# Optimization experiments

Hardware: AMD Instinct MI355X
Metric: run time of the kernel (lower is better)

## Reference

```python
import jax, jax.numpy as jnp
import numpy as np


def setup_inputs() -> dict:
    key = jax.random.key(0)
    k0, k1, k2, k3 = jax.random.split(key, 4)
    B, T, C, H = 4, 4096, 1024, 64
    input_val = jax.random.normal(k0, (B, T, C), dtype=jnp.float32)
    scale = 0.02
    Wq = jax.random.normal(k1, (H, C), dtype=jnp.float32) * scale
    Wk = jax.random.normal(k2, (H, C), dtype=jnp.float32) * scale
    Wv = jax.random.normal(k3, (H, C), dtype=jnp.float32) * scale
    k_mask = jnp.ones((B, T), dtype=jnp.int32)
    return {"input_val": input_val, "Wq": Wq, "Wk": Wk, "Wv": Wv, "k_mask": k_mask}


def reference(input_val, Wq, Wk, Wv, k_mask):
    # input_val: [B, T, C]; Wq/Wk/Wv: [H, C] (torch Linear weight layout)
    B, T, C = input_val.shape
    H = Wq.shape[0]
    Q = input_val @ Wq.T  # [B, T, H]
    K = input_val @ Wk.T  # [B, T, H]
    V = input_val @ Wv.T  # [B, T, H]
    att = jnp.einsum('bqh,bkh->bqk', Q, K) / jnp.sqrt(jnp.asarray(H, input_val.dtype))
    neg_inf = jnp.asarray(-jnp.inf, att.dtype)
    # padding mask over keys: [B, 1, T]
    att = jnp.where(k_mask[:, None, :] == 0, neg_inf, att)
    # causal mask (rebuilt each call in the original)
    causal = jnp.tril(jnp.ones((T, T), dtype=bool))
    att = jnp.where(causal[None, :, :], att, neg_inf)
    att = jax.nn.softmax(att, axis=-1)
    return att @ V  # [B, T, H]
```

## Files before the change

### kernel.cpp

```cpp
#include <hip/hip_runtime.h>

typedef unsigned short u16;
typedef unsigned int u32;
typedef __attribute__((ext_vector_type(4))) float f32x4;
typedef __attribute__((ext_vector_type(8))) short s16x8;
typedef __attribute__((ext_vector_type(4))) int i32x4;
typedef __attribute__((ext_vector_type(2))) u32 u32x2;
typedef __attribute__((ext_vector_type(4))) u32 u32x4;

#define TT 4096
#define NEG_BIG (-3.0e38f)

__device__ __forceinline__ u16 f2bf(float x){
  u32 u = __builtin_bit_cast(u32, x);
  u32 r = (u + 0x7FFFu + ((u >> 16) & 1u)) >> 16;
  return (u16)r;
}
__device__ __forceinline__ u32 pk2(float a, float b){
  return (u32)f2bf(a) | ((u32)f2bf(b) << 16);
}
__device__ __forceinline__ f32x4 mfma16(s16x8 a, s16x8 b, f32x4 c){
  return __builtin_amdgcn_mfma_f32_16x16x32_bf16(a, b, c, 0, 0, 0);
}

__global__ __launch_bounds__(256) void wconv_k(const float* __restrict__ Wq,
                                               const float* __restrict__ Wk,
                                               const float* __restrict__ Wv,
                                               u16* __restrict__ Wb){
  int i = blockIdx.x * 256 + threadIdx.x;
  float v;
  if (i < 65536)       v = Wq[i] * 0.125f;
  else if (i < 131072) v = Wk[i - 65536];
  else                 v = Wv[i - 131072];
  Wb[i] = f2bf(v);
}

__global__ __launch_bounds__(256) void qkv_k(const float* __restrict__ X,
                                             const u16* __restrict__ Wb,
                                             u16* __restrict__ Qb,
                                             u16* __restrict__ Kb,
                                             u16* __restrict__ Vt){
  __shared__ u16 Xs[64][40];
  const int tid = threadIdx.x;
  const int lane = tid & 63;
  const int wid = tid >> 6;
  const int q4 = lane & 15, g = lane >> 4;
  const int row0 = blockIdx.x * 64;
  const int b = row0 >> 12;
  const int trow = row0 & 4095;
  const int srow = tid >> 2, spart = tid & 3;
  const float* xsrc = X + (size_t)(row0 + srow) * 1024 + spart * 8;
  f32x4 c0 = *(const f32x4*)(xsrc);
  f32x4 c1 = *(const f32x4*)(xsrc + 4);
  f32x4 acc[3][4];
  #pragma unroll
  for (int ci = 0; ci < 3; ++ci)
    #pragma unroll
    for (int tt = 0; tt < 4; ++tt) acc[ci][tt] = (f32x4){0.f, 0.f, 0.f, 0.f};
  const int ct0 = wid * 3;

  for (int kc = 0; kc < 32; ++kc){
    s16x8 wf[3];
    #pragma unroll
    for (int ci = 0; ci < 3; ++ci){
      int ct = ct0 + ci;
      wf[ci] = *(const s16x8*)(Wb + (size_t)(ct * 16 + q4) * 1024 + kc * 32 + g * 8);
    }
    const float* nx = xsrc + (kc < 31 ? (kc + 1) * 32 : 0);
    f32x4 n0 = *(const f32x4*)(nx);
    f32x4 n1 = *(const f32x4*)(nx + 4);
    u32x4 wv;
    wv[0] = pk2(c0[0], c0[1]); wv[1] = pk2(c0[2], c0[3]);
    wv[2] = pk2(c1[0], c1[1]); wv[3] = pk2(c1[2], c1[3]);
    *(u32x4*)&Xs[srow][spart * 8] = wv;
    __syncthreads();
    s16x8 xf[4];
    #pragma unroll
    for (int tt = 0; tt < 4; ++tt) xf[tt] = *(const s16x8*)&Xs[tt * 16 + q4][g * 8];
    #pragma unroll
    for (int ci = 0; ci < 3; ++ci){
      #pragma unroll
      for (int tt = 0; tt < 4; ++tt){
        if (ct0 + ci < 8) acc[ci][tt] = mfma16(wf[ci], xf[tt], acc[ci][tt]);
        else              acc[ci][tt] = mfma16(xf[tt], wf[ci], acc[ci][tt]);
      }
    }
    __syncthreads();
    c0 = n0; c1 = n1;
  }
  #pragma unroll
  for (int ci = 0; ci < 3; ++ci){
    int ct = ct0 + ci;
    #pragma unroll
    for (int tt = 0; tt < 4; ++tt){
      f32x4 v = acc[ci][tt];
      u32x2 pw; pw[0] = pk2(v[0], v[1]); pw[1] = pk2(v[2], v[3]);
      if (ct < 8){
        u16* dst = (ct < 4 ? Qb : Kb) + (size_t)(row0 + tt * 16 + q4) * 64 + (ct & 3) * 16 + g * 4;
        *(u32x2*)dst = pw;
      } else {
        u16* dst = Vt + (size_t)(b * 64 + (ct - 8) * 16 + q4) * TT + trow + tt * 16 + g * 4;
        *(u32x2*)dst = pw;
      }
    }
  }
}

__global__ __launch_bounds__(128) void attn_k(const u16* __restrict__ Qb,
                                              const u16* __restrict__ Kb,
                                              const u16* __restrict__ Vt,
                                              const int* __restrict__ km,
                                              float* __restrict__ out){
  __shared__ u16 Plds[2][16][72];
  __shared__ float Part[2][16][64];
  __shared__ float Pml[2][2][16];
  const int tid = threadIdx.x;
  const int wid = tid >> 6;
  const int lane = tid & 63;
  const int q4 = lane & 15, g = lane >> 4;
  const int b = blockIdx.x >> 7;
  const int p = blockIdx.x & 127;
  float mK, lK; f32x4 oK[4];

  #pragma unroll
  for (int si = 0; si < 2; ++si){
    const int s = (si == 0) ? p : 255 - p;
    const int qbase = s * 16;
    const int q_lane = qbase + q4;
    const int ntiles = (s >> 2) + 1;
    const int t0 = (ntiles * wid) >> 1;
    const int t1 = (ntiles * (wid + 1)) >> 1;
    const u16* qptr = Qb + (size_t)(b * TT + qbase + q4) * 64 + g * 8;
    const s16x8 qf0 = *(const s16x8*)(qptr);
    const s16x8 qf1 = *(const s16x8*)(qptr + 32);
    float m = NEG_BIG, l = 0.f;
    f32x4 o[4];
    #pragma unroll
    for (int ht = 0; ht < 4; ++ht) o[ht] = (f32x4){0.f, 0.f, 0.f, 0.f};

    for (int kt = t0; kt < t1; ++kt){
      const int kb = kt * 64;
      const u16* kp = Kb + (size_t)(b * TT + kb + q4) * 64 + g * 8;
      s16x8 kf[4][2];
      #pragma unroll
      for (int mt = 0; mt < 4; ++mt){
        kf[mt][0] = *(const s16x8*)(kp + mt * 1024);
        kf[mt][1] = *(const s16x8*)(kp + mt * 1024 + 32);
      }
      f32x4 sA[4];
      #pragma unroll
      for (int mt = 0; mt < 4; ++mt){
        sA[mt] = mfma16(kf[mt][0], qf0, (f32x4){0.f, 0.f, 0.f, 0.f});
        sA[mt] = mfma16(kf[mt][1], qf1, sA[mt]);
      }
      #pragma unroll
      for (int mt = 0; mt < 4; ++mt){
        i32x4 mk = *(const i32x4*)(km + b * TT + kb + mt * 16 + g * 4);
        #pragma unroll
        for (int r = 0; r < 4; ++r) if (mk[r] == 0) sA[mt][r] = NEG_BIG;
      }
      if (kt == ntiles - 1){
        #pragma unroll
        for (int mt = 0; mt < 4; ++mt)
          #pragma unroll
          for (int r = 0; r < 4; ++r){
            int key = kb + mt * 16 + g * 4 + r;
            if (key > q_lane) sA[mt][r] = NEG_BIG;
          }
      }
      float vmax = NEG_BIG;
      #pragma unroll
      for (int mt = 0; mt < 4; ++mt)
        #pragma unroll
        for (int r = 0; r < 4; ++r) vmax = fmaxf(vmax, sA[mt][r]);
      vmax = fmaxf(vmax, __shfl_xor(vmax, 16));
      vmax = fmaxf(vmax, __shfl_xor(vmax, 32));
      const float mn = fmaxf(m, vmax);
      const float sc = __expf(m - mn);
      float ps = 0.f;
      float pvv[4][4];
      #pragma unroll
      for (int mt = 0; mt < 4; ++mt)
        #pragma unroll
        for (int r = 0; r < 4; ++r){
          float e = __expf(sA[mt][r] - mn);
          pvv[mt][r] = e; ps += e;
        }
      ps += __shfl_xor(ps, 16);
      ps += __shfl_xor(ps, 32);
      l = l * sc + ps;
      m = mn;
      #pragma unroll
      for (int ht = 0; ht < 4; ++ht) o[ht] *= sc;
      #pragma unroll
      for (int mt = 0; mt < 4; ++mt){
        u32x2 pw; pw[0] = pk2(pvv[mt][0], pvv[mt][1]); pw[1] = pk2(pvv[mt][2], pvv[mt][3]);
        *(u32x2*)&Plds[wid][q4][mt * 16 + g * 4] = pw;
      }
      const s16x8 pf0 = *(const s16x8*)&Plds[wid][q4][g * 8];
      const s16x8 pf1 = *(const s16x8*)&Plds[wid][q4][32 + g * 8];
      const u16* vp = Vt + (size_t)(b * 64 + q4) * TT + kb + g * 8;
      #pragma unroll
      for (int ht = 0; ht < 4; ++ht){
        s16x8 vf0 = *(const s16x8*)(vp + (size_t)(ht * 16) * TT);
        s16x8 vf1 = *(const s16x8*)(vp + (size_t)(ht * 16) * TT + 32);
        o[ht] = mfma16(vf0, pf0, o[ht]);
        o[ht] = mfma16(vf1, pf1, o[ht]);
      }
    }
    if (si != wid){
      #pragma unroll
      for (int ht = 0; ht < 4; ++ht) *(f32x4*)&Part[si][q4][ht * 16 + g * 4] = o[ht];
      if (g == 0){ Pml[si][0][q4] = m; Pml[si][1][q4] = l; }
    } else {
      mK = m; lK = l;
      #pragma unroll
      for (int ht = 0; ht < 4; ++ht) oK[ht] = o[ht];
    }
  }
  __syncthreads();
  const int s = (wid == 0) ? p : 255 - p;
  const float m1 = Pml[wid][0][q4], l1 = Pml[wid][1][q4];
  const float mt_ = fmaxf(mK, m1);
  const float a = __expf(mK - mt_), bb = __expf(m1 - mt_);
  const float lt = lK * a + l1 * bb;
  const float rl = 1.0f / lt;
  float* op = out + (size_t)(b * TT + s * 16 + q4) * 64;
  #pragma unroll
  for (int ht = 0; ht < 4; ++ht){
    f32x4 o1 = *(const f32x4*)&Part[wid][q4][ht * 16 + g * 4];
    f32x4 ov;
    #pragma unroll
    for (int r = 0; r < 4; ++r) ov[r] = (oK[ht][r] * a + o1[r] * bb) * rl;
    *(f32x4*)(op + ht * 16 + g * 4) = ov;
  }
}

extern "C" void kernel_launch(void* const* d_in, const int* in_sizes, int n_in,
                              void* d_out, int out_size, void* d_ws, size_t ws_size,
                              hipStream_t stream){
  const float* X  = (const float*)d_in[0];
  const float* Wq = (const float*)d_in[1];
  const float* Wk = (const float*)d_in[2];
  const float* Wv = (const float*)d_in[3];
  const int*   km = (const int*)d_in[4];
  float* out = (float*)d_out;
  u16* Qb = (u16*)d_ws;
  u16* Kb = Qb + (size_t)16384 * 64;
  u16* Vt = Kb + (size_t)16384 * 64;
  u16* Wb = Vt + (size_t)16384 * 64;
  hipLaunchKernelGGL(wconv_k, dim3(768), dim3(256), 0, stream, Wq, Wk, Wv, Wb);
  hipLaunchKernelGGL(qkv_k,   dim3(256), dim3(256), 0, stream, X, Wb, Qb, Kb, Vt);
  hipLaunchKernelGGL(attn_k,  dim3(512), dim3(128), 0, stream, Qb, Kb, Vt, km, out);
}
```

Measured before the change: 223.2 us.

## Split attention key range across 8 waves and halve QKV row tile

The attention kernel now runs 8 waves per block: each of the two query strips is split over 4 waves that each take a quarter of the causal key tiles, and the four partial softmax states are merged through LDS. Previously 2 waves each processed both strips sequentially. The QKV projection kernel processes 32 rows per block instead of 64, doubling its grid to 512 blocks. Both changes aim to raise parallelism and occupancy on the many-CU GPU, at the cost of more LDS, a larger merge step, and less reuse of weight fragments per block in the projection.

After: 192.5 us. 13.8% less time.

```diff
diff --git a/kernel.cpp b/kernel.cpp
--- a/kernel.cpp
+++ b/kernel.cpp
@@ -6,7 +6,6 @@
 typedef __attribute__((ext_vector_type(8))) short s16x8;
 typedef __attribute__((ext_vector_type(4))) int i32x4;
 typedef __attribute__((ext_vector_type(2))) u32 u32x2;
-typedef __attribute__((ext_vector_type(4))) u32 u32x4;
 
 #define TT 4096
 #define NEG_BIG (-3.0e38f)
@@ -40,23 +39,22 @@
                                              u16* __restrict__ Qb,
                                              u16* __restrict__ Kb,
                                              u16* __restrict__ Vt){
-  __shared__ u16 Xs[64][40];
+  __shared__ u16 Xs[32][40];
   const int tid = threadIdx.x;
   const int lane = tid & 63;
   const int wid = tid >> 6;
   const int q4 = lane & 15, g = lane >> 4;
-  const int row0 = blockIdx.x * 64;
+  const int row0 = blockIdx.x * 32;
   const int b = row0 >> 12;
   const int trow = row0 & 4095;
-  const int srow = tid >> 2, spart = tid & 3;
-  const float* xsrc = X + (size_t)(row0 + srow) * 1024 + spart * 8;
+  const int srow = tid >> 3, spart = tid & 7;
+  const float* xsrc = X + (size_t)(row0 + srow) * 1024 + spart * 4;
   f32x4 c0 = *(const f32x4*)(xsrc);
-  f32x4 c1 = *(const f32x4*)(xsrc + 4);
-  f32x4 acc[3][4];
+  f32x4 acc[3][2];
   #pragma unroll
   for (int ci = 0; ci < 3; ++ci)
     #pragma unroll
-    for (int tt = 0; tt < 4; ++tt) acc[ci][tt] = (f32x4){0.f, 0.f, 0.f, 0.f};
+    for (int tt = 0; tt < 2; ++tt) acc[ci][tt] = (f32x4){0.f, 0.f, 0.f, 0.f};
   const int ct0 = wid * 3;
 
   for (int kc = 0; kc < 32; ++kc){
@@ -68,31 +66,29 @@
     }
     const float* nx = xsrc + (kc < 31 ? (kc + 1) * 32 : 0);
     f32x4 n0 = *(const f32x4*)(nx);
-    f32x4 n1 = *(const f32x4*)(nx + 4);
-    u32x4 wv;
+    u32x2 wv;
     wv[0] = pk2(c0[0], c0[1]); wv[1] = pk2(c0[2], c0[3]);
-    wv[2] = pk2(c1[0], c1[1]); wv[3] = pk2(c1[2], c1[3]);
-    *(u32x4*)&Xs[srow][spart * 8] = wv;
+    *(u32x2*)&Xs[srow][spart * 4] = wv;
     __syncthreads();
-    s16x8 xf[4];
-    #pragma unroll
-    for (int tt = 0; tt < 4; ++tt) xf[tt] = *(const s16x8*)&Xs[tt * 16 + q4][g * 8];
+    s16x8 xf[2];
+    #pragma unroll
+    for (int tt = 0; tt < 2; ++tt) xf[tt] = *(const s16x8*)&Xs[tt * 16 + q4][g * 8];
     #pragma unroll
     for (int ci = 0; ci < 3; ++ci){
       #pragma unroll
-      for (int tt = 0; tt < 4; ++tt){
+      for (int tt = 0; tt < 2; ++tt){
         if (ct0 + ci < 8) acc[ci][tt] = mfma16(wf[ci], xf[tt], acc[ci][tt]);
         else              acc[ci][tt] = mfma16(xf[tt], wf[ci], acc[ci][tt]);
       }
     }
     __syncthreads();
-    c0 = n0; c1 = n1;
+    c0 = n0;
   }
   #pragma unroll
   for (int ci = 0; ci < 3; ++ci){
     int ct = ct0 + ci;
     #pragma unroll
-    for (int tt = 0; tt < 4; ++tt){
+    for (int tt = 0; tt < 2; ++tt){
       f32x4 v = acc[ci][tt];
       u32x2 pw; pw[0] = pk2(v[0], v[1]); pw[1] = pk2(v[2], v[3]);
       if (ct < 8){
@@ -106,133 +102,127 @@
   }
 }
 
-__global__ __launch_bounds__(128) void attn_k(const u16* __restrict__ Qb,
-                                              const u16* __restrict__ Kb,
-                                              const u16* __restrict__ Vt,
-                                              const int* __restrict__ km,
-                                              float* __restrict__ out){
-  __shared__ u16 Plds[2][16][72];
-  __shared__ float Part[2][16][64];
-  __shared__ float Pml[2][2][16];
+__global__ __launch_bounds__(512, 4) void attn_k(const u16* __restrict__ Qb,
+                                                 const u16* __restrict__ Kb,
+                                                 const u16* __restrict__ Vt,
+                                                 const int* __restrict__ km,
+                                                 float* __restrict__ out){
+  __shared__ u16 Plds[8][16][72];
+  __shared__ float Part[2][4][16][68];
+  __shared__ float Pml[2][4][2][16];
   const int tid = threadIdx.x;
   const int wid = tid >> 6;
   const int lane = tid & 63;
   const int q4 = lane & 15, g = lane >> 4;
   const int b = blockIdx.x >> 7;
   const int p = blockIdx.x & 127;
-  float mK, lK; f32x4 oK[4];
-
-  #pragma unroll
-  for (int si = 0; si < 2; ++si){
-    const int s = (si == 0) ? p : 255 - p;
-    const int qbase = s * 16;
-    const int q_lane = qbase + q4;
-    const int ntiles = (s >> 2) + 1;
-    const int t0 = (ntiles * wid) >> 1;
-    const int t1 = (ntiles * (wid + 1)) >> 1;
-    const u16* qptr = Qb + (size_t)(b * TT + qbase + q4) * 64 + g * 8;
-    const s16x8 qf0 = *(const s16x8*)(qptr);
-    const s16x8 qf1 = *(const s16x8*)(qptr + 32);
-    float m = NEG_BIG, l = 0.f;
-    f32x4 o[4];
-    #pragma unroll
-    for (int ht = 0; ht < 4; ++ht) o[ht] = (f32x4){0.f, 0.f, 0.f, 0.f};
-
-    for (int kt = t0; kt < t1; ++kt){
-      const int kb = kt * 64;
-      const u16* kp = Kb + (size_t)(b * TT + kb + q4) * 64 + g * 8;
-      s16x8 kf[4][2];
-      #pragma unroll
-      for (int mt = 0; mt < 4; ++mt){
-        kf[mt][0] = *(const s16x8*)(kp + mt * 1024);
-        kf[mt][1] = *(const s16x8*)(kp + mt * 1024 + 32);
-      }
-      f32x4 sA[4];
-      #pragma unroll
-      for (int mt = 0; mt < 4; ++mt){
-        sA[mt] = mfma16(kf[mt][0], qf0, (f32x4){0.f, 0.f, 0.f, 0.f});
-        sA[mt] = mfma16(kf[mt][1], qf1, sA[mt]);
-      }
-      #pragma unroll
-      for (int mt = 0; mt < 4; ++mt){
-        i32x4 mk = *(const i32x4*)(km + b * TT + kb + mt * 16 + g * 4);
-        #pragma unroll
-        for (int r = 0; r < 4; ++r) if (mk[r] == 0) sA[mt][r] = NEG_BIG;
-      }
-      if (kt == ntiles - 1){
-        #pragma unroll
-        for (int mt = 0; mt < 4; ++mt)
-          #pragma unroll
-          for (int r = 0; r < 4; ++r){
-            int key = kb + mt * 16 + g * 4 + r;
-            if (key > q_lane) sA[mt][r] = NEG_BIG;
-          }
-      }
-      float vmax = NEG_BIG;
-      #pragma unroll
-      for (int mt = 0; mt < 4; ++mt)
-        #pragma unroll
-        for (int r = 0; r < 4; ++r) vmax = fmaxf(vmax, sA[mt][r]);
-      vmax = fmaxf(vmax, __shfl_xor(vmax, 16));
-      vmax = fmaxf(vmax, __shfl_xor(vmax, 32));
-      const float mn = fmaxf(m, vmax);
-      const float sc = __expf(m - mn);
-      float ps = 0.f;
-      float pvv[4][4];
+  const int si = wid & 1;
+  const int qt = wid >> 1;
+
+  const int s = (si == 0) ? p : 255 - p;
+  const int qbase = s * 16;
+  const int q_lane = qbase + q4;
+  const int ntiles = (s >> 2) + 1;
+  const int t0 = (ntiles * qt) >> 2;
+  const int t1 = (ntiles * (qt + 1)) >> 2;
+  const u16* qptr = Qb + (size_t)(b * TT + qbase + q4) * 64 + g * 8;
+  const s16x8 qf0 = *(const s16x8*)(qptr);
+  const s16x8 qf1 = *(const s16x8*)(qptr + 32);
+  float m = NEG_BIG, l = 0.f;
+  f32x4 o[4];
+  #pragma unroll
+  for (int ht = 0; ht < 4; ++ht) o[ht] = (f32x4){0.f, 0.f, 0.f, 0.f};
+
+  for (int kt = t0; kt < t1; ++kt){
+    const int kb = kt * 64;
+    const u16* kp = Kb + (size_t)(b * TT + kb + q4) * 64 + g * 8;
+    s16x8 kf[4][2];
+    #pragma unroll
+    for (int mt = 0; mt < 4; ++mt){
+      kf[mt][0] = *(const s16x8*)(kp + mt * 1024);
+      kf[mt][1] = *(const s16x8*)(kp + mt * 1024 + 32);
+    }
+    f32x4 sA[4];
+    #pragma unroll
+    for (int mt = 0; mt < 4; ++mt){
+      sA[mt] = mfma16(kf[mt][0], qf0, (f32x4){0.f, 0.f, 0.f, 0.f});
+      sA[mt] = mfma16(kf[mt][1], qf1, sA[mt]);
+    }
+    #pragma unroll
+    for (int mt = 0; mt < 4; ++mt){
+      i32x4 mk = *(const i32x4*)(km + b * TT + kb + mt * 16 + g * 4);
+      #pragma unroll
+      for (int r = 0; r < 4; ++r) if (mk[r] == 0) sA[mt][r] = NEG_BIG;
+    }
+    if (kt == ntiles - 1){
       #pragma unroll
       for (int mt = 0; mt < 4; ++mt)
         #pragma unroll
         for (int r = 0; r < 4; ++r){
-          float e = __expf(sA[mt][r] - mn);
-          pvv[mt][r] = e; ps += e;
+          int key = kb + mt * 16 + g * 4 + r;
+          if (key > q_lane) sA[mt][r] = NEG_BIG;
         }
-      ps += __shfl_xor(ps, 16);
-      ps += __shfl_xor(ps, 32);
-      l = l * sc + ps;
-      m = mn;
-      #pragma unroll
-      for (int ht = 0; ht < 4; ++ht) o[ht] *= sc;
-      #pragma unroll
-      for (int mt = 0; mt < 4; ++mt){
-        u32x2 pw; pw[0] = pk2(pvv[mt][0], pvv[mt][1]); pw[1] = pk2(pvv[mt][2], pvv[mt][3]);
-        *(u32x2*)&Plds[wid][q4][mt * 16 + g * 4] = pw;
-      }
-      const s16x8 pf0 = *(const s16x8*)&Plds[wid][q4][g * 8];
-      const s16x8 pf1 = *(const s16x8*)&Plds[wid][q4][32 + g * 8];
-      const u16* vp = Vt + (size_t)(b * 64 + q4) * TT + kb + g * 8;
-      #pragma unroll
-      for (int ht = 0; ht < 4; ++ht){
-        s16x8 vf0 = *(const s16x8*)(vp + (size_t)(ht * 16) * TT);
-        s16x8 vf1 = *(const s16x8*)(vp + (size_t)(ht * 16) * TT + 32);
-        o[ht] = mfma16(vf0, pf0, o[ht]);
-        o[ht] = mfma16(vf1, pf1, o[ht]);
-      }
-    }
-    if (si != wid){
-      #pragma unroll
-      for (int ht = 0; ht < 4; ++ht) *(f32x4*)&Part[si][q4][ht * 16 + g * 4] = o[ht];
-      if (g == 0){ Pml[si][0][q4] = m; Pml[si][1][q4] = l; }
-    } else {
-      mK = m; lK = l;
-      #pragma unroll
-      for (int ht = 0; ht < 4; ++ht) oK[ht] = o[ht];
-    }
-  }
+    }
+    float vmax = NEG_BIG;
+    #pragma unroll
+    for (int mt = 0; mt < 4; ++mt)
+      #pragma unroll
+      for (int r = 0; r < 4; ++r) vmax = fmaxf(vmax, sA[mt][r]);
+    vmax = fmaxf(vmax, __shfl_xor(vmax, 16));
+    vmax = fmaxf(vmax, __shfl_xor(vmax, 32));
+    const float mn = fmaxf(m, vmax);
+    const float sc = __expf(m - mn);
+    float ps = 0.f;
+    #pragma unroll
+    for (int mt = 0; mt < 4; ++mt){
+      float e0 = __expf(sA[mt][0] - mn), e1 = __expf(sA[mt][1] - mn);
+      float e2 = __expf(sA[mt][2] - mn), e3 = __expf(sA[mt][3] - mn);
+      ps += (e0 + e1) + (e2 + e3);
+      u32x2 pw; pw[0] = pk2(e0, e1); pw[1] = pk2(e2, e3);
+      *(u32x2*)&Plds[wid][q4][mt * 16 + g * 4] = pw;
+    }
+    ps += __shfl_xor(ps, 16);
+    ps += __shfl_xor(ps, 32);
+    l = l * sc + ps;
+    m = mn;
+    #pragma unroll
+    for (int ht = 0; ht < 4; ++ht) o[ht] *= sc;
+    const s16x8 pf0 = *(const s16x8*)&Plds[wid][q4][g * 8];
+    const s16x8 pf1 = *(const s16x8*)&Plds[wid][q4][32 + g * 8];
+    const u16* vp = Vt + (size_t)(b * 64 + q4) * TT + kb + g * 8;
+    #pragma unroll
+    for (int ht = 0; ht < 4; ++ht){
+      s16x8 vf0 = *(const s16x8*)(vp + (size_t)(ht * 16) * TT);
+      s16x8 vf1 = *(const s16x8*)(vp + (size_t)(ht * 16) * TT + 32);
+      o[ht] = mfma16(vf0, pf0, o[ht]);
+      o[ht] = mfma16(vf1, pf1, o[ht]);
+    }
+  }
+  #pragma unroll
+  for (int ht = 0; ht < 4; ++ht) *(f32x4*)&Part[si][qt][q4][ht * 16 + g * 4] = o[ht];
+  if (g == 0){ Pml[si][qt][0][q4] = m; Pml[si][qt][1][q4] = l; }
   __syncthreads();
-  const int s = (wid == 0) ? p : 255 - p;
-  const float m1 = Pml[wid][0][q4], l1 = Pml[wid][1][q4];
-  const float mt_ = fmaxf(mK, m1);
-  const float a = __expf(mK - mt_), bb = __expf(m1 - mt_);
-  const float lt = lK * a + l1 * bb;
-  const float rl = 1.0f / lt;
-  float* op = out + (size_t)(b * TT + s * 16 + q4) * 64;
-  #pragma unroll
-  for (int ht = 0; ht < 4; ++ht){
-    f32x4 o1 = *(const f32x4*)&Part[wid][q4][ht * 16 + g * 4];
-    f32x4 ov;
-    #pragma unroll
-    for (int r = 0; r < 4; ++r) ov[r] = (oK[ht][r] * a + o1[r] * bb) * rl;
-    *(f32x4*)(op + ht * 16 + g * 4) = ov;
+  if (wid < 2){
+    const int so = (wid == 0) ? p : 255 - p;
+    float mm0 = Pml[wid][0][0][q4], mm1 = Pml[wid][1][0][q4];
+    float mm2 = Pml[wid][2][0][q4], mm3 = Pml[wid][3][0][q4];
+    float ll0 = Pml[wid][0][1][q4], ll1 = Pml[wid][1][1][q4];
+    float ll2 = Pml[wid][2][1][q4], ll3 = Pml[wid][3][1][q4];
+    const float mt_ = fmaxf(fmaxf(mm0, mm1), fmaxf(mm2, mm3));
+    const float w0 = __expf(mm0 - mt_), w1 = __expf(mm1 - mt_);
+    const float w2 = __expf(mm2 - mt_), w3 = __expf(mm3 - mt_);
+    const float lt = ll0 * w0 + ll1 * w1 + ll2 * w2 + ll3 * w3;
+    const float rl = 1.0f / lt;
+    float* op = out + (size_t)(b * TT + so * 16 + q4) * 64;
+    #pragma unroll
+    for (int ht = 0; ht < 4; ++ht){
+      f32x4 o0 = *(const f32x4*)&Part[wid][0][q4][ht * 16 + g * 4];
+      f32x4 o1 = *(const f32x4*)&Part[wid][1][q4][ht * 16 + g * 4];
+      f32x4 o2 = *(const f32x4*)&Part[wid][2][q4][ht * 16 + g * 4];
+      f32x4 o3 = *(const f32x4*)&Part[wid][3][q4][ht * 16 + g * 4];
+      f32x4 ov = (o0 * w0 + o1 * w1 + o2 * w2 + o3 * w3) * rl;
+      *(f32x4*)(op + ht * 16 + g * 4) = ov;
+    }
   }
 }
 
@@ -250,6 +240,6 @@
   u16* Vt = Kb + (size_t)16384 * 64;
   u16* Wb = Vt + (size_t)16384 * 64;
   hipLaunchKernelGGL(wconv_k, dim3(768), dim3(256), 0, stream, Wq, Wk, Wv, Wb);
-  hipLaunchKernelGGL(qkv_k,   dim3(256), dim3(256), 0, stream, X, Wb, Qb, Kb, Vt);
-  hipLaunchKernelGGL(attn_k,  dim3(512), dim3(128), 0, stream, Qb, Kb, Vt, km, out);
-}
+  hipLaunchKernelGGL(qkv_k,   dim3(512), dim3(256), 0, stream, X, Wb, Qb, Kb, Vt);
+  hipLaunchKernelGGL(attn_k,  dim3(512), dim3(512), 0, stream, Qb, Kb, Vt, km, out);
+}
```
